# Optimization experiments

Hardware: AMD Instinct MI355X
Metric: run time of the kernel (lower is better)

## Reference

```python
import jax, jax.numpy as jnp
import numpy as np

B = 4096
D_FULL, D_T1, D_T2 = 1024, 512, 512
N_SPEC, N_SHARED = 4, 4
HID, OUT = 512, 256


def _expert_params(key, n_experts, d_in):
    k1, k2, k3, k4 = jax.random.split(key, 4)
    s1 = 1.0 / np.sqrt(d_in)
    s2 = 1.0 / np.sqrt(HID)
    return {
        'W1': jax.random.uniform(k1, (n_experts, d_in, HID), jnp.float32, -s1, s1),
        'b1': jax.random.uniform(k2, (n_experts, HID), jnp.float32, -s1, s1),
        'W2': jax.random.uniform(k3, (n_experts, HID, OUT), jnp.float32, -s2, s2),
        'b2': jax.random.uniform(k4, (n_experts, OUT), jnp.float32, -s2, s2),
    }


def setup_inputs() -> dict:
    key = jax.random.key(0)
    ks = jax.random.split(key, 12)
    x_full = jax.random.normal(ks[0], (B, D_FULL), jnp.float32)
    x_task1 = jax.random.normal(ks[1], (B, D_T1), jnp.float32)
    x_task2 = jax.random.normal(ks[2], (B, D_T2), jnp.float32)
    ps = _expert_params(ks[3], N_SHARED, D_FULL)
    p1 = _expert_params(ks[4], N_SPEC, D_T1)
    p2 = _expert_params(ks[5], N_SPEC, D_T2)
    sg = 1.0 / np.sqrt(D_FULL)
    s1 = 1.0 / np.sqrt(D_T1)
    s2 = 1.0 / np.sqrt(D_T2)
    return {
        'x_full': x_full, 'x_task1': x_task1, 'x_task2': x_task2,
        'sh_W1': ps['W1'], 'sh_b1': ps['b1'], 'sh_W2': ps['W2'], 'sh_b2': ps['b2'],
        't1_W1': p1['W1'], 't1_b1': p1['b1'], 't1_W2': p1['W2'], 't1_b2': p1['b2'],
        't2_W1': p2['W1'], 't2_b1': p2['b1'], 't2_W2': p2['W2'], 't2_b2': p2['b2'],
        'gsh_W': jax.random.uniform(ks[6], (D_FULL, 2 * N_SPEC + N_SHARED), jnp.float32, -sg, sg),
        'gsh_b': jax.random.uniform(ks[7], (2 * N_SPEC + N_SHARED,), jnp.float32, -sg, sg),
        'g1_W': jax.random.uniform(ks[8], (D_T1, N_SPEC + N_SHARED), jnp.float32, -s1, s1),
        'g1_b': jax.random.uniform(ks[9], (N_SPEC + N_SHARED,), jnp.float32, -s1, s1),
        'g2_W': jax.random.uniform(ks[10], (D_T2, N_SPEC + N_SHARED), jnp.float32, -s2, s2),
        'g2_b': jax.random.uniform(ks[11], (N_SPEC + N_SHARED,), jnp.float32, -s2, s2),
    }


def _experts(x, W1, b1, W2, b2):
    # x: [B, D]; W1: [E, D, H] -> out [E, B, OUT]
    h = jax.nn.relu(jnp.einsum('bd,edh->ebh', x, W1) + b1[:, None, :])
    return jax.nn.relu(jnp.einsum('ebh,eho->ebo', h, W2) + b2[:, None, :])


def reference(x_full, x_task1, x_task2,
              sh_W1, sh_b1, sh_W2, sh_b2,
              t1_W1, t1_b1, t1_W2, t1_b2,
              t2_W1, t2_b1, t2_W2, t2_b2,
              gsh_W, gsh_b, g1_W, g1_b, g2_W, g2_b):
    eo_shared = _experts(x_full, sh_W1, sh_b1, sh_W2, sh_b2)    # [Es, B, OUT]
    eo_t1 = _experts(x_task1, t1_W1, t1_b1, t1_W2, t1_b2)       # [Et, B, OUT]
    eo_t2 = _experts(x_task2, t2_W1, t2_b1, t2_W2, t2_b2)       # [Et, B, OUT]

    g1 = jax.nn.softmax(x_task1 @ g1_W + g1_b, axis=1)          # [B, Et+Es]
    out1 = jnp.einsum('ebc,be->bc', jnp.concatenate([eo_t1, eo_shared], axis=0), g1)

    g2 = jax.nn.softmax(x_task2 @ g2_W + g2_b, axis=1)
    out2 = jnp.einsum('ebc,be->bc', jnp.concatenate([eo_t2, eo_shared], axis=0), g2)

    gsh = jax.nn.softmax(x_full @ gsh_W + gsh_b, axis=1)        # [B, 2Et+Es]
    out_sh = jnp.einsum('ebc,be->bc', jnp.concatenate([eo_t1, eo_t2, eo_shared], axis=0), gsh)

    return (out_sh, out1, out2)
```

## Files before the change

kernel.cpp:

```cpp
#include <hip/hip_runtime.h>

typedef unsigned short u16;
typedef __attribute__((ext_vector_type(8))) short short8;
typedef __attribute__((ext_vector_type(4))) float f32x4;

#define GL2LDS16(src, dst) __builtin_amdgcn_global_load_lds( \
    (const __attribute__((address_space(1))) void*)(src),    \
    (__attribute__((address_space(3))) void*)(dst), 16, 0, 0)

__device__ __forceinline__ u16 f2bf(float f) {
  union { float f; unsigned u; } v; v.f = f;
  unsigned r = v.u + 0x7fffu + ((v.u >> 16) & 1u);
  return (u16)(r >> 16);
}
__device__ __forceinline__ float bf2f(u16 h) {
  union { unsigned u; float f; } v; v.u = ((unsigned)h) << 16; return v.f;
}

__global__ void k_gates_cvt(const float* __restrict__ xf, const float* __restrict__ x1,
                            const float* __restrict__ x2,
                            const float* __restrict__ gshW, const float* __restrict__ gshB,
                            const float* __restrict__ g1W, const float* __restrict__ g1B,
                            const float* __restrict__ g2W, const float* __restrict__ g2B,
                            u16* __restrict__ xfb, u16* __restrict__ x1b, u16* __restrict__ x2b,
                            float* __restrict__ gsh, float* __restrict__ g1o,
                            float* __restrict__ g2o) {
  const int b = blockIdx.x, lane = threadIdx.x;
  float s[12];
#pragma unroll
  for (int j = 0; j < 12; ++j) s[j] = 0.f;
  {
    const float* xr = xf + (size_t)b * 1024;
    u16* xw = xfb + (size_t)b * 1024;
    for (int k = lane; k < 1024; k += 64) {
      float v = xr[k];
      xw[k] = f2bf(v);
      const float* wr = gshW + (size_t)k * 12;
#pragma unroll
      for (int j = 0; j < 12; ++j) s[j] += v * wr[j];
    }
  }
  float u[8], w[8];
#pragma unroll
  for (int j = 0; j < 8; ++j) { u[j] = 0.f; w[j] = 0.f; }
  {
    const float* xr1 = x1 + (size_t)b * 512;
    const float* xr2 = x2 + (size_t)b * 512;
    u16* xw1 = x1b + (size_t)b * 512;
    u16* xw2 = x2b + (size_t)b * 512;
    for (int k = lane; k < 512; k += 64) {
      float v1 = xr1[k], v2 = xr2[k];
      xw1[k] = f2bf(v1); xw2[k] = f2bf(v2);
      const float* w1r = g1W + (size_t)k * 8;
      const float* w2r = g2W + (size_t)k * 8;
#pragma unroll
      for (int j = 0; j < 8; ++j) { u[j] += v1 * w1r[j]; w[j] += v2 * w2r[j]; }
    }
  }
#pragma unroll
  for (int off = 32; off >= 1; off >>= 1) {
#pragma unroll
    for (int j = 0; j < 12; ++j) s[j] += __shfl_xor(s[j], off, 64);
#pragma unroll
    for (int j = 0; j < 8; ++j) { u[j] += __shfl_xor(u[j], off, 64); w[j] += __shfl_xor(w[j], off, 64); }
  }
  if (lane == 0) {
    float m = -1e30f, tot = 0.f;
#pragma unroll
    for (int j = 0; j < 12; ++j) { s[j] += gshB[j]; m = fmaxf(m, s[j]); }
#pragma unroll
    for (int j = 0; j < 12; ++j) { s[j] = __expf(s[j] - m); tot += s[j]; }
    float inv = 1.f / tot;
#pragma unroll
    for (int j = 0; j < 12; ++j) gsh[(size_t)b * 12 + j] = s[j] * inv;
    m = -1e30f; tot = 0.f;
#pragma unroll
    for (int j = 0; j < 8; ++j) { u[j] += g1B[j]; m = fmaxf(m, u[j]); }
#pragma unroll
    for (int j = 0; j < 8; ++j) { u[j] = __expf(u[j] - m); tot += u[j]; }
    inv = 1.f / tot;
#pragma unroll
    for (int j = 0; j < 8; ++j) g1o[(size_t)b * 8 + j] = u[j] * inv;
    m = -1e30f; tot = 0.f;
#pragma unroll
    for (int j = 0; j < 8; ++j) { w[j] += g2B[j]; m = fmaxf(m, w[j]); }
#pragma unroll
    for (int j = 0; j < 8; ++j) { w[j] = __expf(w[j] - m); tot += w[j]; }
    inv = 1.f / tot;
#pragma unroll
    for (int j = 0; j < 8; ++j) g2o[(size_t)b * 8 + j] = w[j] * inv;
  }
}

struct TD { const float* src; u16* dst; int lgTps; int lgNtx; int R; int C; int tileBase; };
struct TArgs { TD d[6]; };

__global__ void k_transpose_all(TArgs ta) {
  __shared__ float tile[32][33];
  const int x = blockIdx.x;
  int di = 0;
#pragma unroll
  for (int i = 1; i < 6; ++i)
    if (x >= ta.d[i].tileBase) di = i;
  TD d = ta.d[di];
  const int local = x - d.tileBase;
  const int slice = local >> d.lgTps;
  const int ti = local & ((1 << d.lgTps) - 1);
  const int tx = ti & ((1 << d.lgNtx) - 1);
  const int ty = ti >> d.lgNtx;
  const float* src = d.src + (size_t)slice * d.R * d.C;
  u16* dst = d.dst + (size_t)slice * d.R * d.C;
  const int c0 = tx * 32, r0 = ty * 32;
  const int ttx = threadIdx.x, tty = threadIdx.y;
#pragma unroll
  for (int i = tty; i < 32; i += 8)
    tile[i][ttx] = src[(size_t)(r0 + i) * d.C + (c0 + ttx)];
  __syncthreads();
#pragma unroll
  for (int i = tty; i < 32; i += 8)
    dst[(size_t)(c0 + i) * d.R + (r0 + ttx)] = f2bf(tile[ttx][i]);
}

struct GemmDesc {
  const u16* A;
  const u16* BT;
  const float* bias;
  u16* C;
  int K;
  int N;
  int iters;
};
struct GemmArgs { GemmDesc d[12]; };

#define PHASE(BUF, KS, MH, ...)                                                   \
  {                                                                               \
    const char* AsB = (const char*)As + (BUF) * 32768;                            \
    const char* BsB = (const char*)Bs + (BUF) * 32768 + (KS) * 16384;             \
    if ((MH) == 0) {                                                              \
      _Pragma("unroll") for (int ni = 0; ni < 4; ++ni)                            \
          b[ni] = *(const short8*)(BsB + boff[ni]);                               \
    }                                                                             \
    _Pragma("unroll") for (int q = 0; q < 4; ++q)                                 \
        a[q] = *(const short8*)(AsB + (aoff[(MH) * 4 + q] ^ ((KS) * 64)));        \
    __VA_ARGS__;                                                                  \
    __builtin_amdgcn_s_barrier();                                                 \
    asm volatile("s_waitcnt lgkmcnt(0)" ::: "memory");                            \
    __builtin_amdgcn_sched_barrier(0);                                            \
    __builtin_amdgcn_s_setprio(1);                                                \
    _Pragma("unroll") for (int q = 0; q < 4; ++q)                                 \
        _Pragma("unroll") for (int ni = 0; ni < 4; ++ni)                          \
            acc[(MH) * 4 + q][ni] = __builtin_amdgcn_mfma_f32_16x16x32_bf16(      \
                a[q], b[ni], acc[(MH) * 4 + q][ni], 0, 0, 0);                     \
    __builtin_amdgcn_s_setprio(0);                                                \
  }

__global__ __launch_bounds__(512, 1) void k_gemm256(GemmArgs args) {
  __shared__ __align__(16) u16 As[32768];
  __shared__ __align__(16) u16 Bs[32768];

  GemmDesc g = args.d[blockIdx.y];
  const int K = g.K, N = g.N, iters = g.iters;
  const int ntN = N >> 8;
  const int lg = (ntN == 2) ? 1 : 0;
  const int bx = blockIdx.x;
  const int row0 = (bx >> lg) << 8;
  const int col0 = (bx & (ntN - 1)) << 8;

  const int tid = threadIdx.x;
  const int lane = tid & 63;
  const int wid = tid >> 6;
  const int wm = wid & 1;
  const int wn = wid >> 1;
  const int lrow = lane & 15;
  const int lkq = lane >> 4;

  int aoff[8], boff[4];
#pragma unroll
  for (int mi = 0; mi < 8; ++mi)
    aoff[mi] = wm * 16384 + (mi * 16 + lrow) * 128 + ((lkq ^ (lrow & 7)) * 16);
#pragma unroll
  for (int ni = 0; ni < 4; ++ni)
    boff[ni] = (wn * 64 + ni * 16 + lrow) * 64 + ((lkq ^ ((lrow >> 1) & 3)) * 16);

  auto stageAhalf = [&](int buf, int half, int kt) {
#pragma unroll
    for (int j = 0; j < 2; ++j) {
      const int cb = (wid * 2 + j) * 64;
      const int c = cb + lane;
      const int r = c >> 3;
      const int cir = (c & 7) ^ (r & 7);
      GL2LDS16(g.A + (size_t)(row0 + half * 128 + r) * K + kt * 64 + cir * 8,
               &As[(buf * 2048 + half * 1024 + cb) * 8]);
    }
  };
  auto stageBhalf = [&](int buf, int ks, int kt) {
#pragma unroll
    for (int j = 0; j < 2; ++j) {
      const int cb = (wid * 2 + j) * 64;
      const int c = cb + lane;
      const int r = c >> 2;
      const int cir = (c & 3) ^ ((r >> 1) & 3);
      GL2LDS16(g.BT + (size_t)(col0 + r) * K + kt * 64 + ks * 32 + cir * 8,
               &Bs[(buf * 2048 + ks * 1024 + cb) * 8]);
    }
  };

  f32x4 acc[8][4];
#pragma unroll
  for (int m = 0; m < 8; ++m)
#pragma unroll
    for (int n = 0; n < 4; ++n)
      acc[m][n] = (f32x4){0.f, 0.f, 0.f, 0.f};

  stageBhalf(0, 0, 0); stageBhalf(0, 1, 0);
  stageAhalf(0, 0, 0); stageAhalf(0, 1, 0);
  stageBhalf(1, 0, 1); stageBhalf(1, 1, 1);
  asm volatile("s_waitcnt vmcnt(4)" ::: "memory");
  __builtin_amdgcn_s_barrier();

  short8 a[4], b[4];
  for (int i = 0; i < iters; ++i) {
    const int t1 = 2 * i + 1;
    const bool nl = (i + 1 < iters);
    PHASE(0, 0, 0, stageAhalf(1, 0, t1));
    __builtin_amdgcn_s_barrier();
    PHASE(0, 0, 1, stageAhalf(1, 1, t1));
    __builtin_amdgcn_s_barrier();
    PHASE(0, 1, 0, if (nl) stageBhalf(0, 0, t1 + 1));
    __builtin_amdgcn_s_barrier();
    PHASE(0, 1, 1, if (nl) stageBhalf(0, 1, t1 + 1));
    if (nl) { asm volatile("s_waitcnt vmcnt(4)" ::: "memory"); }
    else    { asm volatile("s_waitcnt vmcnt(0)" ::: "memory"); }
    __builtin_amdgcn_s_barrier();
    PHASE(1, 0, 0, if (nl) stageAhalf(0, 0, t1 + 1));
    __builtin_amdgcn_s_barrier();
    PHASE(1, 0, 1, if (nl) stageAhalf(0, 1, t1 + 1));
    __builtin_amdgcn_s_barrier();
    PHASE(1, 1, 0, if (nl) stageBhalf(1, 0, t1 + 2));
    __builtin_amdgcn_s_barrier();
    PHASE(1, 1, 1, if (nl) stageBhalf(1, 1, t1 + 2));
    asm volatile("s_waitcnt vmcnt(4)" ::: "memory");
    __builtin_amdgcn_s_barrier();
  }

#pragma unroll
  for (int ni = 0; ni < 4; ++ni) {
    const int gc = col0 + wn * 64 + ni * 16 + lrow;
    const float bv = g.bias[gc];
#pragma unroll
    for (int mi = 0; mi < 8; ++mi) {
      const int gr = row0 + wm * 128 + mi * 16 + lkq * 4;
#pragma unroll
      for (int j = 0; j < 4; ++j) {
        float o = fmaxf(acc[mi][ni][j] + bv, 0.f);
        g.C[(size_t)(gr + j) * N + gc] = f2bf(o);
      }
    }
  }
}

__global__ void k_reduce(const u16* __restrict__ OutB, const float* __restrict__ gsh,
                         const float* __restrict__ g1, const float* __restrict__ g2,
                         float* __restrict__ out) {
  int t = blockIdx.x * 256 + threadIdx.x;
  int b = t >> 5;
  int c0 = (t & 31) << 3;
  float wsh[12], w1[8], w2[8];
#pragma unroll
  for (int j = 0; j < 12; ++j) wsh[j] = gsh[(size_t)b * 12 + j];
#pragma unroll
  for (int j = 0; j < 8; ++j) { w1[j] = g1[(size_t)b * 8 + j]; w2[j] = g2[(size_t)b * 8 + j]; }
  float ash[8] = {0, 0, 0, 0, 0, 0, 0, 0};
  float a1[8] = {0, 0, 0, 0, 0, 0, 0, 0};
  float a2[8] = {0, 0, 0, 0, 0, 0, 0, 0};
#pragma unroll
  for (int e = 0; e < 12; ++e) {
    short8 v = *(const short8*)&OutB[((size_t)e * 4096 + b) * 256 + c0];
    float f[8];
#pragma unroll
    for (int i = 0; i < 8; ++i) f[i] = bf2f((u16)v[i]);
#pragma unroll
    for (int i = 0; i < 8; ++i) ash[i] += wsh[e] * f[i];
    if (e < 4) {
#pragma unroll
      for (int i = 0; i < 8; ++i) a1[i] += w1[e] * f[i];
    } else if (e < 8) {
#pragma unroll
      for (int i = 0; i < 8; ++i) a2[i] += w2[e - 4] * f[i];
    } else {
#pragma unroll
      for (int i = 0; i < 8; ++i) a1[i] += w1[e - 4] * f[i];
#pragma unroll
      for (int i = 0; i < 8; ++i) a2[i] += w2[e - 4] * f[i];
    }
  }
  size_t base = (size_t)b * 256 + c0;
  float4* o;
  o = (float4*)(out + base);
  o[0] = make_float4(ash[0], ash[1], ash[2], ash[3]);
  o[1] = make_float4(ash[4], ash[5], ash[6], ash[7]);
  o = (float4*)(out + 4096ull * 256 + base);
  o[0] = make_float4(a1[0], a1[1], a1[2], a1[3]);
  o[1] = make_float4(a1[4], a1[5], a1[6], a1[7]);
  o = (float4*)(out + 2ull * 4096 * 256 + base);
  o[0] = make_float4(a2[0], a2[1], a2[2], a2[3]);
  o[1] = make_float4(a2[4], a2[5], a2[6], a2[7]);
}

extern "C" void kernel_launch(void* const* d_in, const int* in_sizes, int n_in,
                              void* d_out, int out_size, void* d_ws, size_t ws_size,
                              hipStream_t stream) {
  const float* x_full = (const float*)d_in[0];
  const float* x_t1 = (const float*)d_in[1];
  const float* x_t2 = (const float*)d_in[2];
  const float* sh_W1 = (const float*)d_in[3];
  const float* sh_b1 = (const float*)d_in[4];
  const float* sh_W2 = (const float*)d_in[5];
  const float* sh_b2 = (const float*)d_in[6];
  const float* t1_W1 = (const float*)d_in[7];
  const float* t1_b1 = (const float*)d_in[8];
  const float* t1_W2 = (const float*)d_in[9];
  const float* t1_b2 = (const float*)d_in[10];
  const float* t2_W1 = (const float*)d_in[11];
  const float* t2_b1 = (const float*)d_in[12];
  const float* t2_W2 = (const float*)d_in[13];
  const float* t2_b2 = (const float*)d_in[14];
  const float* gsh_W = (const float*)d_in[15];
  const float* gsh_b = (const float*)d_in[16];
  const float* g1_W = (const float*)d_in[17];
  const float* g1_b = (const float*)d_in[18];
  const float* g2_W = (const float*)d_in[19];
  const float* g2_b = (const float*)d_in[20];

  char* ws = (char*)d_ws;
  size_t off = 0;
  auto alloc = [&](size_t bytes) -> void* {
    void* p = ws + off;
    off += (bytes + 255) & ~(size_t)255;
    return p;
  };
  u16* xf_b = (u16*)alloc(4096ull * 1024 * 2);
  u16* x1_b = (u16*)alloc(4096ull * 512 * 2);
  u16* x2_b = (u16*)alloc(4096ull * 512 * 2);
  u16* w1t_t1 = (u16*)alloc(4ull * 512 * 512 * 2);
  u16* w1t_t2 = (u16*)alloc(4ull * 512 * 512 * 2);
  u16* w1t_sh = (u16*)alloc(4ull * 512 * 1024 * 2);
  u16* w2t = (u16*)alloc(12ull * 256 * 512 * 2);
  u16* H = (u16*)alloc(12ull * 4096 * 512 * 2);
  u16* OutB = (u16*)alloc(12ull * 4096 * 256 * 2);
  float* gshv = (float*)alloc(4096ull * 12 * 4);
  float* g1v = (float*)alloc(4096ull * 8 * 4);
  float* g2v = (float*)alloc(4096ull * 8 * 4);

  k_gates_cvt<<<4096, 64, 0, stream>>>(x_full, x_t1, x_t2, gsh_W, gsh_b, g1_W, g1_b, g2_W, g2_b,
                                       xf_b, x1_b, x2_b, gshv, g1v, g2v);

  TArgs ta;
  ta.d[0] = TD{t1_W1, w1t_t1, 8, 4, 512, 512, 0};
  ta.d[1] = TD{t2_W1, w1t_t2, 8, 4, 512, 512, 1024};
  ta.d[2] = TD{sh_W1, w1t_sh, 9, 4, 1024, 512, 2048};
  ta.d[3] = TD{t1_W2, w2t, 7, 3, 512, 256, 4096};
  ta.d[4] = TD{t2_W2, w2t + 4ull * 256 * 512, 7, 3, 512, 256, 4608};
  ta.d[5] = TD{sh_W2, w2t + 8ull * 256 * 512, 7, 3, 512, 256, 5120};
  k_transpose_all<<<5632, dim3(32, 8), 0, stream>>>(ta);

  GemmArgs ga1;
  for (int e = 0; e < 4; ++e) {
    ga1.d[e] = GemmDesc{xf_b, w1t_sh + (size_t)e * 512 * 1024, sh_b1 + e * 512,
                        H + (size_t)(8 + e) * 4096 * 512, 1024, 512, 8};
    ga1.d[4 + e] = GemmDesc{x1_b, w1t_t1 + (size_t)e * 512 * 512, t1_b1 + e * 512,
                            H + (size_t)e * 4096 * 512, 512, 512, 4};
    ga1.d[8 + e] = GemmDesc{x2_b, w1t_t2 + (size_t)e * 512 * 512, t2_b1 + e * 512,
                            H + (size_t)(4 + e) * 4096 * 512, 512, 512, 4};
  }
  k_gemm256<<<dim3(32, 12), 512, 0, stream>>>(ga1);

  GemmArgs ga2;
  for (int e = 0; e < 12; ++e) {
    const float* bias = (e < 4) ? (t1_b2 + e * 256)
                      : (e < 8) ? (t2_b2 + (e - 4) * 256)
                                : (sh_b2 + (e - 8) * 256);
    ga2.d[e] = GemmDesc{H + (size_t)e * 4096 * 512, w2t + (size_t)e * 256 * 512, bias,
                        OutB + (size_t)e * 4096 * 256, 512, 256, 4};
  }
  k_gemm256<<<dim3(16, 12), 512, 0, stream>>>(ga2);

  k_reduce<<<512, 256, 0, stream>>>(OutB, gshv, g1v, g2v, (float*)d_out);
}
```

Baseline: 113.2 us.

## Swap GEMM operands for vectorized transposed stores and pipeline LDS fragment loads

The GEMM now treats the weights as the M-side operand and the activations as the N-side operand, computing the transposed product. Each lane's four accumulator values then sit in consecutive output columns, so the epilogue writes them as one 8-byte packed store with a float4 bias load instead of four scalar 2-byte stores. The main loop is also restructured with double-buffered register fragments (cur/next) and partial lgkmcnt waits, so LDS reads for the next MFMA block overlap the current MFMA block. This adds register pressure and more barriers, and its correctness relies on the grid decode (bx>>4, bx&15) matching the tile counts.

```diff
diff --git a/kernel.cpp b/kernel.cpp
--- a/kernel.cpp
+++ b/kernel.cpp
@@ -122,49 +122,51 @@
 }
 
 struct GemmDesc {
-  const u16* A;
-  const u16* BT;
+  const u16* W;
+  const u16* X;
   const float* bias;
-  u16* C;
+  u16* Ct;
   int K;
-  int N;
+  int M;
   int iters;
 };
 struct GemmArgs { GemmDesc d[12]; };
 
-#define PHASE(BUF, KS, MH, ...)                                                   \
-  {                                                                               \
-    const char* AsB = (const char*)As + (BUF) * 32768;                            \
-    const char* BsB = (const char*)Bs + (BUF) * 32768 + (KS) * 16384;             \
-    if ((MH) == 0) {                                                              \
-      _Pragma("unroll") for (int ni = 0; ni < 4; ++ni)                            \
-          b[ni] = *(const short8*)(BsB + boff[ni]);                               \
-    }                                                                             \
-    _Pragma("unroll") for (int q = 0; q < 4; ++q)                                 \
-        a[q] = *(const short8*)(AsB + (aoff[(MH) * 4 + q] ^ ((KS) * 64)));        \
-    __VA_ARGS__;                                                                  \
-    __builtin_amdgcn_s_barrier();                                                 \
-    asm volatile("s_waitcnt lgkmcnt(0)" ::: "memory");                            \
-    __builtin_amdgcn_sched_barrier(0);                                            \
-    __builtin_amdgcn_s_setprio(1);                                                \
-    _Pragma("unroll") for (int q = 0; q < 4; ++q)                                 \
-        _Pragma("unroll") for (int ni = 0; ni < 4; ++ni)                          \
-            acc[(MH) * 4 + q][ni] = __builtin_amdgcn_mfma_f32_16x16x32_bf16(      \
-                a[q], b[ni], acc[(MH) * 4 + q][ni], 0, 0, 0);                     \
-    __builtin_amdgcn_s_setprio(0);                                                \
-  }
+#define LDA4(DST, BUF, KS, MH)                                                  \
+  _Pragma("unroll") for (int q = 0; q < 4; ++q)                                 \
+      DST[q] = *(const short8*)((const char*)As + (BUF) * 32768 +               \
+                                (aoff[(MH) * 4 + q] ^ ((KS) * 64)));
+
+#define LDB4(DST, BUF, KS)                                                      \
+  _Pragma("unroll") for (int n = 0; n < 4; ++n)                                 \
+      DST[n] = *(const short8*)((const char*)Bs + (BUF) * 32768 +               \
+                                (KS) * 16384 + boff[n]);
+
+#define MFMA16(AF, BF, MH)                                                      \
+  __builtin_amdgcn_s_setprio(1);                                                \
+  _Pragma("unroll") for (int q = 0; q < 4; ++q)                                 \
+      _Pragma("unroll") for (int n = 0; n < 4; ++n)                             \
+          acc[(MH) * 4 + q][n] = __builtin_amdgcn_mfma_f32_16x16x32_bf16(       \
+              AF[q], BF[n], acc[(MH) * 4 + q][n], 0, 0, 0);                     \
+  __builtin_amdgcn_s_setprio(0);
+
+#define BARR __builtin_amdgcn_s_barrier()
+#define WAITL(N)                                                 \
+  {                                                              \
+    asm volatile("s_waitcnt lgkmcnt(" #N ")" ::: "memory");      \
+    __builtin_amdgcn_sched_barrier(0);                           \
+  }
+#define WAITV(N) asm volatile("s_waitcnt vmcnt(" #N ")" ::: "memory")
 
 __global__ __launch_bounds__(512, 1) void k_gemm256(GemmArgs args) {
   __shared__ __align__(16) u16 As[32768];
   __shared__ __align__(16) u16 Bs[32768];
 
   GemmDesc g = args.d[blockIdx.y];
-  const int K = g.K, N = g.N, iters = g.iters;
-  const int ntN = N >> 8;
-  const int lg = (ntN == 2) ? 1 : 0;
+  const int K = g.K, M = g.M, iters = g.iters;
   const int bx = blockIdx.x;
-  const int row0 = (bx >> lg) << 8;
-  const int col0 = (bx & (ntN - 1)) << 8;
+  const int row0 = (bx >> 4) << 8;
+  const int col0 = (bx & 15) << 8;
 
   const int tid = threadIdx.x;
   const int lane = tid & 63;
@@ -189,7 +191,7 @@
       const int c = cb + lane;
       const int r = c >> 3;
       const int cir = (c & 7) ^ (r & 7);
-      GL2LDS16(g.A + (size_t)(row0 + half * 128 + r) * K + kt * 64 + cir * 8,
+      GL2LDS16(g.W + (size_t)(row0 + half * 128 + r) * K + kt * 64 + cir * 8,
                &As[(buf * 2048 + half * 1024 + cb) * 8]);
     }
   };
@@ -200,7 +202,7 @@
       const int c = cb + lane;
       const int r = c >> 2;
       const int cir = (c & 3) ^ ((r >> 1) & 3);
-      GL2LDS16(g.BT + (size_t)(col0 + r) * K + kt * 64 + ks * 32 + cir * 8,
+      GL2LDS16(g.X + (size_t)(col0 + r) * K + kt * 64 + ks * 32 + cir * 8,
                &Bs[(buf * 2048 + ks * 1024 + cb) * 8]);
     }
   };
@@ -215,46 +217,53 @@
   stageBhalf(0, 0, 0); stageBhalf(0, 1, 0);
   stageAhalf(0, 0, 0); stageAhalf(0, 1, 0);
   stageBhalf(1, 0, 1); stageBhalf(1, 1, 1);
-  asm volatile("s_waitcnt vmcnt(4)" ::: "memory");
-  __builtin_amdgcn_s_barrier();
-
-  short8 a[4], b[4];
+  WAITV(4);
+  BARR;
+
+  short8 a_cur[4], a_nxt[4], b_cur[4], b_nxt[4];
   for (int i = 0; i < iters; ++i) {
     const int t1 = 2 * i + 1;
     const bool nl = (i + 1 < iters);
-    PHASE(0, 0, 0, stageAhalf(1, 0, t1));
-    __builtin_amdgcn_s_barrier();
-    PHASE(0, 0, 1, stageAhalf(1, 1, t1));
-    __builtin_amdgcn_s_barrier();
-    PHASE(0, 1, 0, if (nl) stageBhalf(0, 0, t1 + 1));
-    __builtin_amdgcn_s_barrier();
-    PHASE(0, 1, 1, if (nl) stageBhalf(0, 1, t1 + 1));
-    if (nl) { asm volatile("s_waitcnt vmcnt(4)" ::: "memory"); }
-    else    { asm volatile("s_waitcnt vmcnt(0)" ::: "memory"); }
-    __builtin_amdgcn_s_barrier();
-    PHASE(1, 0, 0, if (nl) stageAhalf(0, 0, t1 + 1));
-    __builtin_amdgcn_s_barrier();
-    PHASE(1, 0, 1, if (nl) stageAhalf(0, 1, t1 + 1));
-    __builtin_amdgcn_s_barrier();
-    PHASE(1, 1, 0, if (nl) stageBhalf(1, 0, t1 + 2));
-    __builtin_amdgcn_s_barrier();
-    PHASE(1, 1, 1, if (nl) stageBhalf(1, 1, t1 + 2));
-    asm volatile("s_waitcnt vmcnt(4)" ::: "memory");
-    __builtin_amdgcn_s_barrier();
-  }
-
-#pragma unroll
-  for (int ni = 0; ni < 4; ++ni) {
-    const int gc = col0 + wn * 64 + ni * 16 + lrow;
-    const float bv = g.bias[gc];
-#pragma unroll
-    for (int mi = 0; mi < 8; ++mi) {
-      const int gr = row0 + wm * 128 + mi * 16 + lkq * 4;
-#pragma unroll
-      for (int j = 0; j < 4; ++j) {
-        float o = fmaxf(acc[mi][ni][j] + bv, 0.f);
-        g.C[(size_t)(gr + j) * N + gc] = f2bf(o);
-      }
+    LDB4(b_cur, 0, 0); LDA4(a_cur, 0, 0, 0); LDA4(a_nxt, 0, 0, 1);
+    stageAhalf(1, 0, t1);
+    BARR; WAITL(4); MFMA16(a_cur, b_cur, 0); BARR;
+    LDB4(b_nxt, 0, 1); LDA4(a_cur, 0, 1, 0);
+    stageAhalf(1, 1, t1);
+    BARR; WAITL(8); MFMA16(a_nxt, b_cur, 1); BARR;
+    LDA4(a_nxt, 0, 1, 1);
+    if (nl) stageBhalf(0, 0, t1 + 1);
+    BARR; WAITL(4); MFMA16(a_cur, b_nxt, 0); BARR;
+    if (nl) stageBhalf(0, 1, t1 + 1);
+    BARR; WAITL(0); MFMA16(a_nxt, b_nxt, 1);
+    if (nl) { WAITV(4); } else { WAITV(0); }
+    BARR;
+    LDB4(b_cur, 1, 0); LDA4(a_cur, 1, 0, 0); LDA4(a_nxt, 1, 0, 1);
+    if (nl) stageAhalf(0, 0, t1 + 1);
+    BARR; WAITL(4); MFMA16(a_cur, b_cur, 0); BARR;
+    LDB4(b_nxt, 1, 1); LDA4(a_cur, 1, 1, 0);
+    if (nl) stageAhalf(0, 1, t1 + 1);
+    BARR; WAITL(8); MFMA16(a_nxt, b_cur, 1); BARR;
+    LDA4(a_nxt, 1, 1, 1);
+    if (nl) stageBhalf(1, 0, t1 + 2);
+    BARR; WAITL(4); MFMA16(a_cur, b_nxt, 0); BARR;
+    if (nl) stageBhalf(1, 1, t1 + 2);
+    BARR; WAITL(0); MFMA16(a_nxt, b_nxt, 1);
+    WAITV(4);
+    BARR;
+  }
+
+#pragma unroll
+  for (int mi = 0; mi < 8; ++mi) {
+    const int gr = row0 + wm * 128 + mi * 16 + lkq * 4;
+    const float4 bv = *(const float4*)(g.bias + gr);
+#pragma unroll
+    for (int ni = 0; ni < 4; ++ni) {
+      const int gc = col0 + wn * 64 + ni * 16 + lrow;
+      unsigned lo = (unsigned)f2bf(fmaxf(acc[mi][ni][0] + bv.x, 0.f)) |
+                    ((unsigned)f2bf(fmaxf(acc[mi][ni][1] + bv.y, 0.f)) << 16);
+      unsigned hi = (unsigned)f2bf(fmaxf(acc[mi][ni][2] + bv.z, 0.f)) |
+                    ((unsigned)f2bf(fmaxf(acc[mi][ni][3] + bv.w, 0.f)) << 16);
+      *(uint2*)(g.Ct + (size_t)gc * M + gr) = make_uint2(lo, hi);
     }
   }
 }
@@ -366,11 +375,11 @@
 
   GemmArgs ga1;
   for (int e = 0; e < 4; ++e) {
-    ga1.d[e] = GemmDesc{xf_b, w1t_sh + (size_t)e * 512 * 1024, sh_b1 + e * 512,
+    ga1.d[e] = GemmDesc{w1t_sh + (size_t)e * 512 * 1024, xf_b, sh_b1 + e * 512,
                         H + (size_t)(8 + e) * 4096 * 512, 1024, 512, 8};
-    ga1.d[4 + e] = GemmDesc{x1_b, w1t_t1 + (size_t)e * 512 * 512, t1_b1 + e * 512,
+    ga1.d[4 + e] = GemmDesc{w1t_t1 + (size_t)e * 512 * 512, x1_b, t1_b1 + e * 512,
                             H + (size_t)e * 4096 * 512, 512, 512, 4};
-    ga1.d[8 + e] = GemmDesc{x2_b, w1t_t2 + (size_t)e * 512 * 512, t2_b1 + e * 512,
+    ga1.d[8 + e] = GemmDesc{w1t_t2 + (size_t)e * 512 * 512, x2_b, t2_b1 + e * 512,
                             H + (size_t)(4 + e) * 4096 * 512, 512, 512, 4};
   }
   k_gemm256<<<dim3(32, 12), 512, 0, stream>>>(ga1);
@@ -380,7 +389,7 @@
     const float* bias = (e < 4) ? (t1_b2 + e * 256)
                       : (e < 8) ? (t2_b2 + (e - 4) * 256)
                                 : (sh_b2 + (e - 8) * 256);
-    ga2.d[e] = GemmDesc{H + (size_t)e * 4096 * 512, w2t + (size_t)e * 256 * 512, bias,
+    ga2.d[e] = GemmDesc{w2t + (size_t)e * 256 * 512, H + (size_t)e * 4096 * 512, bias,
                         OutB + (size_t)e * 4096 * 256, 512, 256, 4};
   }
   k_gemm256<<<dim3(16, 12), 512, 0, stream>>>(ga2);
```

After: 123.4 us. +9.0%, slower.
